# Optimization experiments

Measured on AMD Instinct MI355X. Metric: run time of the kernel, lower is better.

## Reference

```python
import jax, jax.numpy as jnp
import numpy as np

B = 256
N = 256


def setup_inputs() -> dict:
    key = jax.random.key(0)
    ks = jax.random.split(key, 6)
    X = jax.random.normal(ks[0], (B, N), dtype=jnp.float32)
    context = jax.random.normal(ks[1], (B, N), dtype=jnp.float32)
    W = jax.random.normal(ks[2], (N, N), dtype=jnp.float32) * 0.1
    scale = jnp.ones((1,), dtype=jnp.float32)
    A = jax.random.uniform(ks[3], (N, N), dtype=jnp.float32)
    cl_weight = jax.random.normal(ks[4], (N * N, N), dtype=jnp.float32) * 0.02
    cl_bias = jax.random.normal(ks[5], (N * N,), dtype=jnp.float32) * 0.02
    t = 3
    return {"X": X, "context": context, "W": W, "scale": scale, "A": A,
            "cl_weight": cl_weight, "cl_bias": cl_bias, "t": t}


def reference(X, context, W, scale, A, cl_weight, cl_bias, t):
    # context_L path: context-conditioned adjustment of W, shape [B, N, N]
    Bsz, n = X.shape
    adjust = (context @ cl_weight.T + cl_bias).reshape(Bsz, n, n)
    W_new = adjust + W  # broadcast [N,N] over batch
    # diag term: sum over rows i of (W_new @ A)[b, i, k] = einsum bij,jk->bk
    d = jnp.einsum('bij,jk->bk', W_new, A)
    eye = jnp.eye(n, dtype=X.dtype)
    L = d[:, :, None] * eye - W_new          # diag_embed(d) - W_new, [B,N,N]
    new_context = context * (t / (t + 1)) + X / (t + 1)
    L_T = scale * jnp.swapaxes(L, -1, -2)    # [B,N,N]
    update = jnp.einsum('bn,bnm->bm', X, L_T)  # matmul(X[...,None,:], L_T).squeeze()
    return (update, new_context)
```

## Files before the change

kernel.cpp:

```cpp
#include <hip/hip_runtime.h>

#define N 256
#define NN 65536

typedef __attribute__((ext_vector_type(8))) __bf16 bf16x8;
typedef __attribute__((ext_vector_type(4))) __bf16 bf16x4v;
typedef __attribute__((ext_vector_type(4))) float f32x4;

#define F_PART   0u
#define F_SPART  2097152u
#define F_WSC    2621440u
#define F_SFULL  2621696u
#define F_YADJ   2687232u
#define WS_FLOATS 2752768u

static __device__ __forceinline__ f32x4 mfma16(bf16x8 a, bf16x8 b, f32x4 c) {
  return __builtin_amdgcn_mfma_f32_16x16x32_bf16(a, b, c, 0, 0, 0);
}
static __device__ __forceinline__ bf16x4v pack4(float4 v) {
  bf16x4v r;
  r[0] = (__bf16)v.x; r[1] = (__bf16)v.y; r[2] = (__bf16)v.z; r[3] = (__bf16)v.w;
  return r;
}
static __device__ __forceinline__ bf16x8 pack8(float4 a, float4 b) {
  bf16x8 r;
  r[0] = (__bf16)a.x; r[1] = (__bf16)a.y; r[2] = (__bf16)a.z; r[3] = (__bf16)a.w;
  r[4] = (__bf16)b.x; r[5] = (__bf16)b.y; r[6] = (__bf16)b.z; r[7] = (__bf16)b.w;
  return r;
}

#define BARL()                                                            \
  asm volatile("s_waitcnt lgkmcnt(0)" ::: "memory");                      \
  __builtin_amdgcn_s_barrier();                                           \
  __builtin_amdgcn_sched_barrier(0);

__global__ void __launch_bounds__(256, 2) kbig(
    const float* __restrict__ X, const float* __restrict__ ctx,
    const float* __restrict__ W, const float* __restrict__ clb,
    const float* __restrict__ clw, float* __restrict__ ws)
{
  extern __shared__ char smem[];
  float* xl   = (float*)(smem + 49152);
  float* sred = (float*)(smem + 53248);
  float* red  = (float*)smem;
  const int t = threadIdx.x;
  const int bh = blockIdx.x >> 8;
  const int rem = blockIdx.x & 255;
  const int mt = rem >> 5, s = rem & 31;
  const int n0 = s * 8, m0g = mt * 32, b0g = bh * 128;

  const int lane = t & 63, w = t >> 6;
  const int wb = w * 32;
  const int l15 = lane & 15, lhi = lane >> 4;
  const int swz = (l15 & 7) << 4;
  const float4* clwf4 = (const float4*)clw;

  bf16x8 af[2][8];
#pragma unroll
  for (int i = 0; i < 2; ++i)
#pragma unroll
    for (int c = 0; c < 8; ++c) {
      const float4* p = (const float4*)(ctx + (b0g + wb + i * 16 + l15) * N +
                                        c * 32 + lhi * 8);
      af[i][c] = pack8(p[0], p[1]);
    }
  if (t < 128) {
    const float4* xp = (const float4*)(X + (b0g + t) * N + n0);
    const float4 x0 = xp[0], x1 = xp[1];
    xl[0 * 128 + t] = x0.x; xl[1 * 128 + t] = x0.y;
    xl[2 * 128 + t] = x0.z; xl[3 * 128 + t] = x0.w;
    xl[4 * 128 + t] = x1.x; xl[5 * 128 + t] = x1.y;
    xl[6 * 128 + t] = x1.z; xl[7 * 128 + t] = x1.w;
  }

#define ISSUE(TT, R)                                                        \
  _Pragma("unroll")                                                         \
  for (int i = 0; i < 8; ++i) {                                             \
    const int rowl = w * 8 + i;                                             \
    R[i] = clwf4[(size_t)((m0g + rowl) * 256 + n0 + (TT)) * 64 + lane];     \
  }
#define WRITE(TT, R)                                                        \
  _Pragma("unroll")                                                         \
  for (int i = 0; i < 8; ++i) {                                             \
    const int rowl = w * 8 + i;                                             \
    *(bf16x4v*)(smem + ((TT) % 3) * 16384 + rowl * 512 +                    \
                ((lane * 8) ^ ((rowl & 7) << 4))) = pack4(R[i]);            \
  }

  float4 rA[8], rB[8];
  ISSUE(0, rA)
  ISSUE(1, rB)
  __builtin_amdgcn_sched_barrier(0);

  const f32x4 zero = {0.f, 0.f, 0.f, 0.f};
  f32x4 acc[2][2];
  acc[0][0] = zero; acc[0][1] = zero; acc[1][0] = zero; acc[1][1] = zero;

#define COMP(NNV)                                                           \
  {                                                                         \
    const char* buf = smem + ((NNV) % 3) * 16384;                           \
    f32x4 h[2][2];                                                          \
    h[0][0] = zero; h[0][1] = zero; h[1][0] = zero; h[1][1] = zero;         \
    _Pragma("unroll")                                                       \
    for (int c = 0; c < 8; ++c) {                                           \
      const int kb = c * 64 + lhi * 16;                                     \
      bf16x8 b0 = *(const bf16x8*)(buf + l15 * 512 + (kb ^ swz));           \
      bf16x8 b1 = *(const bf16x8*)(buf + (16 + l15) * 512 + (kb ^ swz));    \
      h[0][0] = mfma16(af[0][c], b0, h[0][0]);                              \
      h[0][1] = mfma16(af[0][c], b1, h[0][1]);                              \
      h[1][0] = mfma16(af[1][c], b0, h[1][0]);                              \
      h[1][1] = mfma16(af[1][c], b1, h[1][1]);                              \
    }                                                                       \
    _Pragma("unroll")                                                       \
    for (int fb = 0; fb < 2; ++fb) {                                        \
      _Pragma("unroll")                                                     \
      for (int r = 0; r < 4; ++r) {                                         \
        const int brow = wb + fb * 16 + lhi * 4 + r;                        \
        const float xv = xl[(NNV) * 128 + brow];                            \
        acc[fb][0][r] += xv * h[fb][0][r];                                  \
        acc[fb][1][r] += xv * h[fb][1][r];                                  \
        float v = h[fb][0][r] + h[fb][1][r];                                \
        v += __shfl_xor(v, 1); v += __shfl_xor(v, 2);                       \
        v += __shfl_xor(v, 4); v += __shfl_xor(v, 8);                       \
        if (l15 == 0) sred[(NNV) * 128 + brow] = v;                         \
      }                                                                     \
    }                                                                       \
  }

  WRITE(0, rA)
  BARL();
  ISSUE(2, rA) __builtin_amdgcn_sched_barrier(0); WRITE(1, rB) BARL(); COMP(0)
  ISSUE(3, rB) __builtin_amdgcn_sched_barrier(0); WRITE(2, rA) BARL(); COMP(1)
  ISSUE(4, rA) __builtin_amdgcn_sched_barrier(0); WRITE(3, rB) BARL(); COMP(2)
  ISSUE(5, rB) __builtin_amdgcn_sched_barrier(0); WRITE(4, rA) BARL(); COMP(3)
  ISSUE(6, rA) __builtin_amdgcn_sched_barrier(0); WRITE(5, rB) BARL(); COMP(4)
  ISSUE(7, rB) __builtin_amdgcn_sched_barrier(0); WRITE(6, rA) BARL(); COMP(5)
  WRITE(7, rB) BARL(); COMP(6)
  COMP(7)
#undef ISSUE
#undef WRITE
#undef COMP

  const int base = blockIdx.x * 4096;
#pragma unroll
  for (int fb = 0; fb < 2; ++fb)
#pragma unroll
    for (int fm = 0; fm < 2; ++fm)
#pragma unroll
      for (int r = 0; r < 4; ++r)
        ws[F_PART + base + (wb + fb * 16 + lhi * 4 + r) * 32 + fm * 16 + l15] =
            acc[fb][fm][r];

  {
    const int bl = wb + (lane >> 1);
    const int nh = (lane & 1) * 4;
    float4 v;
    v.x = sred[(nh + 0) * 128 + bl];
    v.y = sred[(nh + 1) * 128 + bl];
    v.z = sred[(nh + 2) * 128 + bl];
    v.w = sred[(nh + 3) * 128 + bl];
    *(float4*)(ws + F_SPART + mt * NN + (b0g + bl) * N + n0 + nh) = v;
  }

  if (mt == 0 && bh == 0) {
    __syncthreads();
    const float4* wp = (const float4*)(W + t * N + s * 8);
    const float4* cp = (const float4*)(clb + t * N + s * 8);
    const float4 a0 = wp[0], a1 = wp[1], c0 = cp[0], c1 = cp[1];
    red[0 * 256 + t] = a0.x + c0.x; red[1 * 256 + t] = a0.y + c0.y;
    red[2 * 256 + t] = a0.z + c0.z; red[3 * 256 + t] = a0.w + c0.w;
    red[4 * 256 + t] = a1.x + c1.x; red[5 * 256 + t] = a1.y + c1.y;
    red[6 * 256 + t] = a1.z + c1.z; red[7 * 256 + t] = a1.w + c1.w;
    __syncthreads();
    if (t < 64) {
      const int jj = t >> 3, seg = t & 7;
      float v = 0.f;
#pragma unroll
      for (int i = 0; i < 32; ++i) v += red[jj * 256 + seg * 32 + i];
      v += __shfl_xor(v, 1);
      v += __shfl_xor(v, 2);
      v += __shfl_xor(v, 4);
      if (seg == 0) ws[F_WSC + s * 8 + jj] = v;
    }
  }
}

__global__ void __launch_bounds__(256) kred(float* __restrict__ ws)
{
  const int o = blockIdx.x * 256 + threadIdx.x;
  const int b = o >> 8, col = o & 255;
  const int mt = col >> 5, ml = col & 31;
  const int bhh = b >> 7, bl = b & 127;
  float y = 0.f;
#pragma unroll
  for (int si = 0; si < 32; ++si)
    y += ws[F_PART + (bhh * 256 + mt * 32 + si) * 4096 + bl * 32 + ml];
  ws[F_YADJ + o] = y;
  float sv = ws[F_WSC + col];
#pragma unroll
  for (int q = 0; q < 8; ++q)
    sv += ws[F_SPART + q * NN + o];
  ws[F_SFULL + o] = sv;
}

__global__ void __launch_bounds__(256) kfin(
    const float* __restrict__ X, const float* __restrict__ ctx,
    const float* __restrict__ W, const float* __restrict__ clb,
    const float* __restrict__ A, const float* __restrict__ scale,
    const int* __restrict__ tptr, float* __restrict__ out,
    float* __restrict__ ws)
{
  extern __shared__ char smem[];
  const int t = threadIdx.x, blk = blockIdx.x;
  const int b0 = (blk >> 3) * 32, k0 = (blk & 7) * 32;
  {
    const int row = t >> 3, q = t & 7;
    const int sw = (row & 7) << 4;
    const float4* sp = (const float4*)(ws + F_SFULL + (b0 + row) * N);
    const float4* xp = (const float4*)(X + (b0 + row) * N);
    const float4* wp = (const float4*)(W + (k0 + row) * N);
    const float4* cp = (const float4*)(clb + (k0 + row) * N);
#pragma unroll
    for (int i = 0; i < 8; ++i) {
      const int f4 = q * 8 + i;
      const int off = row * 512 + ((f4 * 8) ^ sw);
      *(bf16x4v*)(smem + off) = pack4(sp[f4]);
      *(bf16x4v*)(smem + 16384 + off) = pack4(xp[f4]);
      const float4 wv = wp[f4], cv = cp[f4];
      float4 s2;
      s2.x = wv.x + cv.x; s2.y = wv.y + cv.y;
      s2.z = wv.z + cv.z; s2.w = wv.w + cv.w;
      *(bf16x4v*)(smem + 49152 + off) = pack4(s2);
    }
    const float4* ap = (const float4*)(A + t * N + k0);
    char* at = smem + 32768;
#pragma unroll
    for (int i = 0; i < 8; ++i) {
      const float4 v = ap[i];
      const int kk = i * 4;
      *(__bf16*)(at + (kk + 0) * 512 + ((t * 2) ^ (((kk + 0) & 7) << 4))) = (__bf16)v.x;
      *(__bf16*)(at + (kk + 1) * 512 + ((t * 2) ^ (((kk + 1) & 7) << 4))) = (__bf16)v.y;
      *(__bf16*)(at + (kk + 2) * 512 + ((t * 2) ^ (((kk + 2) & 7) << 4))) = (__bf16)v.z;
      *(__bf16*)(at + (kk + 3) * 512 + ((t * 2) ^ (((kk + 3) & 7) << 4))) = (__bf16)v.w;
    }
  }
  __syncthreads();
  const int lane = t & 63, w = t >> 6;
  const int l15 = lane & 15, lhi = lane >> 4;
  const int wqb = (w >> 1) * 16, wqk = (w & 1) * 16;
  const int swz = (l15 & 7) << 4;
  f32x4 accd = {0.f, 0.f, 0.f, 0.f}, accw = {0.f, 0.f, 0.f, 0.f};
#pragma unroll
  for (int c = 0; c < 8; ++c) {
    const int kb = c * 64 + lhi * 16;
    bf16x8 as  = *(const bf16x8*)(smem + (wqb + l15) * 512 + (kb ^ swz));
    bf16x8 aat = *(const bf16x8*)(smem + 32768 + (wqk + l15) * 512 + (kb ^ swz));
    bf16x8 ax  = *(const bf16x8*)(smem + 16384 + (wqb + l15) * 512 + (kb ^ swz));
    bf16x8 awc = *(const bf16x8*)(smem + 49152 + (wqk + l15) * 512 + (kb ^ swz));
    accd = mfma16(as, aat, accd);
    accw = mfma16(ax, awc, accw);
  }
  const float sc = scale[0];
  const float tf = (float)(*tptr);
  const float c1 = tf / (tf + 1.f), c2 = 1.f / (tf + 1.f);
#pragma unroll
  for (int r = 0; r < 4; ++r) {
    const int b = b0 + wqb + lhi * 4 + r, k = k0 + wqk + l15;
    const int idx = b * N + k;
    const float xv = X[idx];
    out[idx] = sc * (xv * accd[r] - accw[r] - ws[F_YADJ + idx]);
    out[NN + idx] = ctx[idx] * c1 + xv * c2;
  }
}

extern "C" void kernel_launch(void* const* d_in, const int* in_sizes, int n_in,
                              void* d_out, int out_size, void* d_ws, size_t ws_size,
                              hipStream_t stream)
{
  (void)in_sizes; (void)n_in; (void)out_size;
  const float* X     = (const float*)d_in[0];
  const float* ctx   = (const float*)d_in[1];
  const float* W     = (const float*)d_in[2];
  const float* scale = (const float*)d_in[3];
  const float* A     = (const float*)d_in[4];
  const float* clw   = (const float*)d_in[5];
  const float* clb   = (const float*)d_in[6];
  const int*   tptr  = (const int*)d_in[7];
  float* out = (float*)d_out;
  float* ws  = (float*)d_ws;

  if (ws_size < (size_t)WS_FLOATS * sizeof(float)) return;

  (void)hipFuncSetAttribute((const void*)kbig,
                            hipFuncAttributeMaxDynamicSharedMemorySize, 57344);
  (void)hipFuncSetAttribute((const void*)kfin,
                            hipFuncAttributeMaxDynamicSharedMemorySize, 65536);

  kbig<<<512, 256, 57344, stream>>>(X, ctx, W, clb, clw, ws);
  kred<<<256, 256, 0, stream>>>(ws);
  kfin<<<64, 256, 65536, stream>>>(X, ctx, W, clb, A, scale, tptr, out, ws);
}
```

Measured before the change: 53.07 us.

## Compute row-sum term via column-summed cl_weight and separate small GEMM

Drops the per-stage shuffle reductions that built the row-sum term S inside the big GEMM. Instead, blocks with bh==0 sum cl_weight over the 32 m rows of each tile while staging it, which gives a column-summed weight matrix. kred converts that matrix to bf16 and a new kred2 kernel multiplies it by context with MFMA. The main loop also goes from a triple-buffered, software-prefetched pipeline to a simpler double-buffered stage-then-compute loop. This cuts shuffle work and LDS use but loses the load/compute overlap and adds another kernel launch.

Result: slower. 56.83 us (+7.1%).

```diff
diff --git a/kernel.cpp b/kernel.cpp
--- a/kernel.cpp
+++ b/kernel.cpp
@@ -8,11 +8,12 @@
 typedef __attribute__((ext_vector_type(4))) float f32x4;
 
 #define F_PART   0u
-#define F_SPART  2097152u
+#define F_CSPART 2097152u
 #define F_WSC    2621440u
-#define F_SFULL  2621696u
-#define F_YADJ   2687232u
-#define WS_FLOATS 2752768u
+#define F_CSB    2621696u
+#define F_SFULL  2654464u
+#define F_YADJ   2720000u
+#define WS_FLOATS 2785536u
 
 static __device__ __forceinline__ f32x4 mfma16(bf16x8 a, bf16x8 b, f32x4 c) {
   return __builtin_amdgcn_mfma_f32_16x16x32_bf16(a, b, c, 0, 0, 0);
@@ -34,15 +35,15 @@
   __builtin_amdgcn_s_barrier();                                           \
   __builtin_amdgcn_sched_barrier(0);
 
-__global__ void __launch_bounds__(256, 2) kbig(
+__global__ void __launch_bounds__(256) kbig(
     const float* __restrict__ X, const float* __restrict__ ctx,
     const float* __restrict__ W, const float* __restrict__ clb,
     const float* __restrict__ clw, float* __restrict__ ws)
 {
   extern __shared__ char smem[];
-  float* xl   = (float*)(smem + 49152);
-  float* sred = (float*)(smem + 53248);
-  float* red  = (float*)smem;
+  float* csl = (float*)(smem + 32768);
+  float* xl  = (float*)(smem + 40960);
+  float* red = (float*)smem;
   const int t = threadIdx.x;
   const int bh = blockIdx.x >> 8;
   const int rem = blockIdx.x & 255;
@@ -73,32 +74,39 @@
     xl[6 * 128 + t] = x1.z; xl[7 * 128 + t] = x1.w;
   }
 
-#define ISSUE(TT, R)                                                        \
-  _Pragma("unroll")                                                         \
-  for (int i = 0; i < 8; ++i) {                                             \
-    const int rowl = w * 8 + i;                                             \
-    R[i] = clwf4[(size_t)((m0g + rowl) * 256 + n0 + (TT)) * 64 + lane];     \
-  }
-#define WRITE(TT, R)                                                        \
-  _Pragma("unroll")                                                         \
-  for (int i = 0; i < 8; ++i) {                                             \
-    const int rowl = w * 8 + i;                                             \
-    *(bf16x4v*)(smem + ((TT) % 3) * 16384 + rowl * 512 +                    \
-                ((lane * 8) ^ ((rowl & 7) << 4))) = pack4(R[i]);            \
-  }
-
-  float4 rA[8], rB[8];
-  ISSUE(0, rA)
-  ISSUE(1, rB)
-  __builtin_amdgcn_sched_barrier(0);
-
   const f32x4 zero = {0.f, 0.f, 0.f, 0.f};
   f32x4 acc[2][2];
   acc[0][0] = zero; acc[0][1] = zero; acc[1][0] = zero; acc[1][1] = zero;
 
+#define STAGE(TT)                                                           \
+  {                                                                         \
+    float4 r[8];                                                            \
+    _Pragma("unroll")                                                       \
+    for (int i = 0; i < 8; ++i) {                                           \
+      const int rowl = w * 8 + i;                                           \
+      r[i] = clwf4[(size_t)((m0g + rowl) * 256 + n0 + (TT)) * 64 + lane];   \
+    }                                                                       \
+    _Pragma("unroll")                                                       \
+    for (int i = 0; i < 8; ++i) {                                           \
+      const int rowl = w * 8 + i;                                           \
+      *(bf16x4v*)(smem + ((TT) & 1) * 16384 + rowl * 512 +                  \
+                  ((lane * 8) ^ ((rowl & 7) << 4))) = pack4(r[i]);          \
+    }                                                                       \
+    if (bh == 0) {                                                          \
+      float4 cso = r[0];                                                    \
+      _Pragma("unroll")                                                     \
+      for (int i = 1; i < 8; ++i) {                                         \
+        cso.x += r[i].x; cso.y += r[i].y;                                   \
+        cso.z += r[i].z; cso.w += r[i].w;                                   \
+      }                                                                     \
+      *(float4*)(csl + ((TT) & 1) * 1024 + w * 256 + lane * 4) = cso;       \
+    }                                                                       \
+    BARL();                                                                 \
+  }
+
 #define COMP(NNV)                                                           \
   {                                                                         \
-    const char* buf = smem + ((NNV) % 3) * 16384;                           \
+    const char* buf = smem + ((NNV) & 1) * 16384;                           \
     f32x4 h[2][2];                                                          \
     h[0][0] = zero; h[0][1] = zero; h[1][0] = zero; h[1][1] = zero;         \
     _Pragma("unroll")                                                       \
@@ -115,30 +123,28 @@
     for (int fb = 0; fb < 2; ++fb) {                                        \
       _Pragma("unroll")                                                     \
       for (int r = 0; r < 4; ++r) {                                         \
-        const int brow = wb + fb * 16 + lhi * 4 + r;                        \
-        const float xv = xl[(NNV) * 128 + brow];                            \
+        const float xv = xl[(NNV) * 128 + wb + fb * 16 + lhi * 4 + r];      \
         acc[fb][0][r] += xv * h[fb][0][r];                                  \
         acc[fb][1][r] += xv * h[fb][1][r];                                  \
-        float v = h[fb][0][r] + h[fb][1][r];                                \
-        v += __shfl_xor(v, 1); v += __shfl_xor(v, 2);                       \
-        v += __shfl_xor(v, 4); v += __shfl_xor(v, 8);                       \
-        if (l15 == 0) sred[(NNV) * 128 + brow] = v;                         \
       }                                                                     \
     }                                                                       \
-  }
-
-  WRITE(0, rA)
-  BARL();
-  ISSUE(2, rA) __builtin_amdgcn_sched_barrier(0); WRITE(1, rB) BARL(); COMP(0)
-  ISSUE(3, rB) __builtin_amdgcn_sched_barrier(0); WRITE(2, rA) BARL(); COMP(1)
-  ISSUE(4, rA) __builtin_amdgcn_sched_barrier(0); WRITE(3, rB) BARL(); COMP(2)
-  ISSUE(5, rB) __builtin_amdgcn_sched_barrier(0); WRITE(4, rA) BARL(); COMP(3)
-  ISSUE(6, rA) __builtin_amdgcn_sched_barrier(0); WRITE(5, rB) BARL(); COMP(4)
-  ISSUE(7, rB) __builtin_amdgcn_sched_barrier(0); WRITE(6, rA) BARL(); COMP(5)
-  WRITE(7, rB) BARL(); COMP(6)
-  COMP(7)
-#undef ISSUE
-#undef WRITE
+    if (bh == 0) {                                                          \
+      const int cb = ((NNV) & 1) * 1024;                                    \
+      float cv = csl[cb + t] + csl[cb + 256 + t] +                          \
+                 csl[cb + 512 + t] + csl[cb + 768 + t];                     \
+      ws[F_CSPART + mt * 65536u + (n0 + (NNV)) * 256 + t] = cv;             \
+    }                                                                       \
+  }
+
+  STAGE(0) COMP(0)
+  STAGE(1) COMP(1)
+  STAGE(2) COMP(2)
+  STAGE(3) COMP(3)
+  STAGE(4) COMP(4)
+  STAGE(5) COMP(5)
+  STAGE(6) COMP(6)
+  STAGE(7) COMP(7)
+#undef STAGE
 #undef COMP
 
   const int base = blockIdx.x * 4096;
@@ -150,17 +156,6 @@
       for (int r = 0; r < 4; ++r)
         ws[F_PART + base + (wb + fb * 16 + lhi * 4 + r) * 32 + fm * 16 + l15] =
             acc[fb][fm][r];
-
-  {
-    const int bl = wb + (lane >> 1);
-    const int nh = (lane & 1) * 4;
-    float4 v;
-    v.x = sred[(nh + 0) * 128 + bl];
-    v.y = sred[(nh + 1) * 128 + bl];
-    v.z = sred[(nh + 2) * 128 + bl];
-    v.w = sred[(nh + 3) * 128 + bl];
-    *(float4*)(ws + F_SPART + mt * NN + (b0g + bl) * N + n0 + nh) = v;
-  }
 
   if (mt == 0 && bh == 0) {
     __syncthreads();
@@ -196,11 +191,40 @@
   for (int si = 0; si < 32; ++si)
     y += ws[F_PART + (bhh * 256 + mt * 32 + si) * 4096 + bl * 32 + ml];
   ws[F_YADJ + o] = y;
-  float sv = ws[F_WSC + col];
+  float cv = 0.f;
 #pragma unroll
   for (int q = 0; q < 8; ++q)
-    sv += ws[F_SPART + q * NN + o];
-  ws[F_SFULL + o] = sv;
+    cv += ws[F_CSPART + q * 65536u + o];
+  ((__bf16*)(ws + F_CSB))[o] = (__bf16)cv;
+}
+
+__global__ void __launch_bounds__(256) kred2(
+    const float* __restrict__ ctx, float* __restrict__ ws)
+{
+  const int t = threadIdx.x, blk = blockIdx.x;
+  const int b0 = (blk >> 3) * 32, j0 = (blk & 7) * 32;
+  const int lane = t & 63, w = t >> 6;
+  const int l15 = lane & 15, lhi = lane >> 4;
+  const int wqb = (w >> 1) * 16, wqj = (w & 1) * 16;
+  const char* csb = (const char*)(ws + F_CSB);
+
+  f32x4 accq = {0.f, 0.f, 0.f, 0.f};
+#pragma unroll
+  for (int c = 0; c < 8; ++c) {
+    const float4* p = (const float4*)(ctx + (b0 + wqb + l15) * N +
+                                      c * 32 + lhi * 8);
+    bf16x8 a = pack8(p[0], p[1]);
+    bf16x8 b = *(const bf16x8*)(csb + (j0 + wqj + l15) * 512 +
+                                c * 64 + lhi * 16);
+    accq = mfma16(a, b, accq);
+  }
+  const int j = j0 + wqj + l15;
+  const float wscv = ws[F_WSC + j];
+#pragma unroll
+  for (int r = 0; r < 4; ++r) {
+    const int b = b0 + wqb + lhi * 4 + r;
+    ws[F_SFULL + b * N + j] = accq[r] + wscv;
+  }
 }
 
 __global__ void __launch_bounds__(256) kfin(
@@ -292,11 +316,12 @@
   if (ws_size < (size_t)WS_FLOATS * sizeof(float)) return;
 
   (void)hipFuncSetAttribute((const void*)kbig,
-                            hipFuncAttributeMaxDynamicSharedMemorySize, 57344);
+                            hipFuncAttributeMaxDynamicSharedMemorySize, 45056);
   (void)hipFuncSetAttribute((const void*)kfin,
                             hipFuncAttributeMaxDynamicSharedMemorySize, 65536);
 
-  kbig<<<512, 256, 57344, stream>>>(X, ctx, W, clb, clw, ws);
+  kbig<<<512, 256, 45056, stream>>>(X, ctx, W, clb, clw, ws);
   kred<<<256, 256, 0, stream>>>(ws);
+  kred2<<<64, 256, 0, stream>>>(ctx, ws);
   kfin<<<64, 256, 65536, stream>>>(X, ctx, W, clb, A, scale, tptr, out, ws);
 }
```
